# Kernel optimization log

Measured on AMD Instinct MI355X. Metric: run time of the kernel, lower is better.

## Reference

```python
import jax, jax.numpy as jnp
import numpy as np

B, S, D = 4, 8192, 1024
H, DH = 16, 64  # n_heads = d_model // d_head
SCALE = DH ** -0.5


def setup_inputs() -> dict:
    key = jax.random.key(0)
    ks = jax.random.split(key, 4)
    x = jax.random.normal(ks[0], (B, S, D), dtype=jnp.float32)
    Wq = jax.random.normal(ks[1], (D, D), dtype=jnp.float32) * 0.02
    Wkv = jax.random.normal(ks[2], (D, 2 * D), dtype=jnp.float32) * 0.02
    Wlin = jax.random.normal(ks[3], (D, D), dtype=jnp.float32) * 0.02
    blin = jnp.zeros((D,), dtype=jnp.float32)
    return {"x": x, "Wq": Wq, "Wkv": Wkv, "Wlin": Wlin, "blin": blin}


def reference(x, Wq, Wkv, Wlin, blin):
    # Q projection: [B,S,D] -> [B,H,S,DH]
    Q = (x @ Wq).reshape(B, S, H, DH).transpose(0, 2, 1, 3)
    # KV projection: output reshaped per-head as 2*DH then split (matches
    # torch unflatten(-1,(H,2*DH)).chunk(2,-1) interleaving)
    KV = (x @ Wkv).reshape(B, S, H, 2 * DH).transpose(0, 2, 1, 3)  # [B,H,S,2*DH]
    K, V = KV[..., :DH], KV[..., DH:]
    # linear attention: softmax Q over feature dim, K over sequence dim
    Q = jax.nn.softmax(Q, axis=-1) * SCALE
    K = jax.nn.softmax(K, axis=-2)
    # context = K^T @ V : [B,H,DH,DH] (avoids O(S^2) score matrix)
    ctx = jnp.einsum('bhsd,bhse->bhde', K, V)
    out = jnp.einsum('bhsd,bhde->bhse', Q, ctx)  # [B,H,S,DH]
    out = out.transpose(0, 2, 1, 3).reshape(B, S, D)
    return out @ Wlin + blin
```

## Files before the change

### kernel.cpp

```cpp
#include <hip/hip_runtime.h>
#include <cstdint>
#include <cstddef>

typedef unsigned short u16;
typedef unsigned int u32;
typedef __attribute__((ext_vector_type(8))) __bf16 bf16x8;
typedef __attribute__((ext_vector_type(4))) float f32x4;
typedef __attribute__((ext_vector_type(2))) unsigned int u32x2;
typedef __attribute__((ext_vector_type(8))) unsigned short u16x8;
typedef __attribute__((ext_vector_type(4))) unsigned short u16x4;

__device__ __forceinline__ u16 f2bf(float f) {
  union { float f; unsigned u; } v; v.f = f;
  unsigned r = v.u + 0x7fffu + ((v.u >> 16) & 1u);
  return (u16)(r >> 16);
}
__device__ __forceinline__ float bf2f(u16 x) {
  union { float f; unsigned u; } v; v.u = ((unsigned)x) << 16;
  return v.f;
}
__device__ __forceinline__ u32 pk2(float a, float b) {
  union { float f; unsigned u; } x, y; x.f = a; y.f = b;
  unsigned ra = x.u + 0x7fffu + ((x.u >> 16) & 1u);
  unsigned rb = y.u + 0x7fffu + ((y.u >> 16) & 1u);
  return (ra >> 16) | (rb & 0xffff0000u);
}

__device__ __forceinline__ void gll16(const void* g, void* l) {
  __builtin_amdgcn_global_load_lds(
      (const __attribute__((address_space(1))) void*)g,
      (__attribute__((address_space(3))) void*)l, 16, 0, 0);
}

__global__ __launch_bounds__(256) void cvt_x(const float* __restrict__ x,
                                             u16* __restrict__ xb, int n) {
  int i = (blockIdx.x * 256 + threadIdx.x) * 4;
  if (i < n) {
    f32x4 v = __builtin_nontemporal_load((const f32x4*)(x + i));
    u16x4 o = { f2bf(v[0]), f2bf(v[1]), f2bf(v[2]), f2bf(v[3]) };
    *(u16x4*)(xb + i) = o;
  }
}

__global__ __launch_bounds__(256) void build_w3t(const float* __restrict__ Wq,
                                                 const float* __restrict__ Wkv,
                                                 u16* __restrict__ W3t) {
  __shared__ float tile[32][33];
  int bx = blockIdx.x, by = blockIdx.y;
  int tx = threadIdx.x & 31, tyb = threadIdx.x >> 5;
  int n = bx * 32 + tx;
  int u = n & 63;
  int nl = (n & ~63) | ((u & 15) << 2) | (u >> 4);
  const float* src; int scol, sld;
  if (nl < 1024)      { src = Wq;  scol = nl;                                  sld = 1024; }
  else if (nl < 2048) { int m = nl - 1024; src = Wkv; scol = (m >> 6) * 128 + (m & 63);      sld = 2048; }
  else                { int m = nl - 2048; src = Wkv; scol = (m >> 6) * 128 + 64 + (m & 63); sld = 2048; }
#pragma unroll
  for (int i = 0; i < 4; ++i) {
    int k = by * 32 + tyb + i * 8;
    tile[tyb + i * 8][tx] = src[(size_t)k * sld + scol];
  }
  __syncthreads();
#pragma unroll
  for (int i = 0; i < 4; ++i) {
    int n2 = bx * 32 + tyb + i * 8;
    int k2 = by * 32 + tx;
    W3t[(size_t)n2 * 1024 + k2] = f2bf(tile[tx][tyb + i * 8]);
  }
}

template <int MODE>
__global__ __launch_bounds__(512, 2)
void gemm_bt_k(const u16* __restrict__ A, int lda,
               const u16* __restrict__ Bt0, int ldb, int K,
               u16* __restrict__ Lout, int ldc,
               float* __restrict__ Fout,
               float* __restrict__ Zp, const float* __restrict__ bias,
               size_t bstride, int rows_per_batch) {
  __shared__ __align__(16) char sm[131072];
  const int tid  = threadIdx.x;
  const int lane = tid & 63, w = tid >> 6;
  const int wm = w >> 2, wn = w & 3;

  const int nbx = gridDim.x;
  const int nby = gridDim.y;
  const int o = blockIdx.y * nbx + blockIdx.x;
  const int x = o & 7, j = o >> 3;
  const int CM = nby >> 2, CN = nbx >> 1;
  const int jn = j % CN, jm = j / CN;
  const int tileM = ((x >> 1) * CM + jm) * 256;
  const int tileN = ((x & 1) * CN + jn) * 256;

  const u16* Bt = Bt0;
  if (MODE == 2) Bt += (size_t)(tileM / rows_per_batch) * bstride;

  const int r0 = tid >> 3;
  const int pp = (tid & 7) ^ (r0 & 7);
  const u16* gA = A  + (size_t)(tileM + r0) * lda + pp * 8;
  const u16* gB = Bt + (size_t)(tileN + r0) * ldb + pp * 8;
  char* smw = sm + w * 1024;

  const int cl = lane & 15, q = lane >> 4;
  int roA[8], roB[4];
#pragma unroll
  for (int mi = 0; mi < 8; ++mi) roA[mi] = (wm * 128 + mi * 16 + cl) * 128;
#pragma unroll
  for (int ni = 0; ni < 4; ++ni) roB[ni] = (wn * 64 + ni * 16 + cl) * 128;
  const int ck0 = ((0 + q) ^ (cl & 7)) * 16;
  const int ck1 = ((4 + q) ^ (cl & 7)) * 16;

  f32x4 acc[8][4];
#pragma unroll
  for (int i = 0; i < 8; ++i)
#pragma unroll
    for (int j2 = 0; j2 < 4; ++j2) acc[i][j2] = (f32x4){0.f, 0.f, 0.f, 0.f};

  bf16x8 ra[4][2], rb0[2][2], rb1[2][2];

#define FENCE asm volatile("" ::: "memory")
#define STG(ab, g, ld_, bufb, h, kc) do {                                        \
    gll16((g) + (size_t)(h) * 128 * (ld_) + (kc),                                \
          smw + (bufb) + (ab) * 32768 + (h) * 16384);                            \
    gll16((g) + ((size_t)(h) * 128 + 64) * (ld_) + (kc),                         \
          smw + (bufb) + (ab) * 32768 + (h) * 16384 + 8192);                     \
  } while (0)

  const int NT = K >> 6;

  STG(0, gA, lda, 0, 0, 0);
  STG(1, gB, ldb, 0, 0, 0);
  STG(0, gA, lda, 0, 1, 0);
  STG(1, gB, ldb, 0, 1, 0);
  if (NT > 1) {
    STG(0, gA, lda, 65536, 0, 64);
    STG(1, gB, ldb, 65536, 0, 64);
    STG(0, gA, lda, 65536, 1, 64);
    asm volatile("s_waitcnt vmcnt(6)" ::: "memory");
  } else {
    asm volatile("s_waitcnt vmcnt(0)" ::: "memory");
  }
  FENCE; __builtin_amdgcn_s_barrier(); FENCE;

  for (int kt = 0; kt < NT; ++kt) {
    const int bufb  = (kt & 1) << 16;
    const int nbufb = bufb ^ 65536;
    const char* sA = sm + bufb;
    const char* sB = sm + bufb + 32768;

#pragma unroll
    for (int mi = 0; mi < 4; ++mi) {
      ra[mi][0] = *(const bf16x8*)(sA + roA[mi] + ck0);
      ra[mi][1] = *(const bf16x8*)(sA + roA[mi] + ck1);
    }
#pragma unroll
    for (int ni = 0; ni < 2; ++ni) {
      rb0[ni][0] = *(const bf16x8*)(sB + roB[ni] + ck0);
      rb0[ni][1] = *(const bf16x8*)(sB + roB[ni] + ck1);
      rb1[ni][0] = *(const bf16x8*)(sB + roB[2 + ni] + ck0);
      rb1[ni][1] = *(const bf16x8*)(sB + roB[2 + ni] + ck1);
    }
    if (kt + 1 < NT) STG(1, gB, ldb, nbufb, 1, (kt + 1) * 64);
    __builtin_amdgcn_s_setprio(1);
#pragma unroll
    for (int mi = 0; mi < 4; ++mi)
#pragma unroll
      for (int ni = 0; ni < 2; ++ni) {
        acc[mi][ni] = __builtin_amdgcn_mfma_f32_16x16x32_bf16(ra[mi][0], rb0[ni][0], acc[mi][ni], 0, 0, 0);
        acc[mi][ni] = __builtin_amdgcn_mfma_f32_16x16x32_bf16(ra[mi][1], rb0[ni][1], acc[mi][ni], 0, 0, 0);
      }
#pragma unroll
    for (int mi = 0; mi < 4; ++mi)
#pragma unroll
      for (int ni = 0; ni < 2; ++ni) {
        acc[mi][2 + ni] = __builtin_amdgcn_mfma_f32_16x16x32_bf16(ra[mi][0], rb1[ni][0], acc[mi][2 + ni], 0, 0, 0);
        acc[mi][2 + ni] = __builtin_amdgcn_mfma_f32_16x16x32_bf16(ra[mi][1], rb1[ni][1], acc[mi][2 + ni], 0, 0, 0);
      }
    __builtin_amdgcn_s_setprio(0);
    FENCE; __builtin_amdgcn_s_barrier(); FENCE;

#pragma unroll
    for (int mi = 0; mi < 4; ++mi) {
      ra[mi][0] = *(const bf16x8*)(sA + roA[4 + mi] + ck0);
      ra[mi][1] = *(const bf16x8*)(sA + roA[4 + mi] + ck1);
    }
    if (kt + 2 < NT) STG(1, gB, ldb, bufb, 0, (kt + 2) * 64);
    __builtin_amdgcn_s_setprio(1);
#pragma unroll
    for (int mi = 0; mi < 4; ++mi)
#pragma unroll
      for (int ni = 0; ni < 2; ++ni) {
        acc[4 + mi][2 + ni] = __builtin_amdgcn_mfma_f32_16x16x32_bf16(ra[mi][0], rb1[ni][0], acc[4 + mi][2 + ni], 0, 0, 0);
        acc[4 + mi][2 + ni] = __builtin_amdgcn_mfma_f32_16x16x32_bf16(ra[mi][1], rb1[ni][1], acc[4 + mi][2 + ni], 0, 0, 0);
      }
    __builtin_amdgcn_s_setprio(0);
    FENCE; __builtin_amdgcn_s_barrier(); FENCE;

    if (kt + 2 < NT) {
      STG(0, gA, lda, bufb, 0, (kt + 2) * 64);
      STG(0, gA, lda, bufb, 1, (kt + 2) * 64);
    }
    __builtin_amdgcn_s_setprio(1);
#pragma unroll
    for (int mi = 0; mi < 4; ++mi)
#pragma unroll
      for (int ni = 0; ni < 2; ++ni) {
        acc[4 + mi][ni] = __builtin_amdgcn_mfma_f32_16x16x32_bf16(ra[mi][0], rb0[ni][0], acc[4 + mi][ni], 0, 0, 0);
        acc[4 + mi][ni] = __builtin_amdgcn_mfma_f32_16x16x32_bf16(ra[mi][1], rb0[ni][1], acc[4 + mi][ni], 0, 0, 0);
      }
    __builtin_amdgcn_s_setprio(0);
    if (kt + 2 < NT) asm volatile("s_waitcnt vmcnt(6)" ::: "memory");
    else             asm volatile("s_waitcnt vmcnt(0)" ::: "memory");
    FENCE; __builtin_amdgcn_s_barrier(); FENCE;
  }
#undef STG
#undef FENCE

  const int colBase = tileN + wn * 64;
  const int rowBase = tileM + wm * 128;

  if (MODE == 1) {
    if (colBase < 1024) {
#pragma unroll
      for (int mi = 0; mi < 8; ++mi) {
#pragma unroll
        for (int r = 0; r < 4; ++r) {
          float e0 = __expf(acc[mi][0][r]), e1 = __expf(acc[mi][1][r]);
          float e2 = __expf(acc[mi][2][r]), e3 = __expf(acc[mi][3][r]);
          float s = (e0 + e1) + (e2 + e3);
          s += __shfl_xor(s, 1); s += __shfl_xor(s, 2);
          s += __shfl_xor(s, 4); s += __shfl_xor(s, 8);
          float inv = 0.125f / s;
          int row = rowBase + mi * 16 + q * 4 + r;
          u32x2 pv = { pk2(e0 * inv, e1 * inv), pk2(e2 * inv, e3 * inv) };
          __builtin_nontemporal_store(pv, (u32x2*)(Lout + (size_t)row * ldc + colBase + cl * 4));
        }
      }
    } else if (colBase < 2048) {
      float zp0 = 0.f, zp1 = 0.f, zp2 = 0.f, zp3 = 0.f;
      const int b = tileM / rows_per_batch;
#pragma unroll
      for (int mi = 0; mi < 8; ++mi) {
#pragma unroll
        for (int r = 0; r < 4; ++r) {
          float e0 = __expf(acc[mi][0][r]), e1 = __expf(acc[mi][1][r]);
          float e2 = __expf(acc[mi][2][r]), e3 = __expf(acc[mi][3][r]);
          zp0 += e0; zp1 += e1; zp2 += e2; zp3 += e3;
          int row = rowBase + mi * 16 + q * 4 + r;
          u32x2 pv = { pk2(e0, e1), pk2(e2, e3) };
          __builtin_nontemporal_store(pv, (u32x2*)(Lout + (size_t)row * ldc + colBase + cl * 4));
        }
      }
      float zp[4] = { zp0, zp1, zp2, zp3 };
#pragma unroll
      for (int ni = 0; ni < 4; ++ni) {
        float z = zp[ni];
        z += __shfl_xor(z, 16);
        z += __shfl_xor(z, 32);
        if (q == 0) atomicAdd(&Zp[b * 1024 + (colBase - 1024) + cl * 4 + ni], z);
      }
    } else {
#pragma unroll
      for (int mi = 0; mi < 8; ++mi) {
#pragma unroll
        for (int r = 0; r < 4; ++r) {
          int row = rowBase + mi * 16 + q * 4 + r;
          u32x2 pv = { pk2(acc[mi][0][r], acc[mi][1][r]),
                       pk2(acc[mi][2][r], acc[mi][3][r]) };
          __builtin_nontemporal_store(pv, (u32x2*)(Lout + (size_t)row * ldc + colBase + cl * 4));
        }
      }
    }
  } else {
    const float4 bb = *(const float4*)(bias + colBase + cl * 4);
#pragma unroll
    for (int mi = 0; mi < 8; ++mi) {
#pragma unroll
      for (int r = 0; r < 4; ++r) {
        int row = rowBase + mi * 16 + q * 4 + r;
        f32x4 v = { acc[mi][0][r] + bb.x, acc[mi][1][r] + bb.y,
                    acc[mi][2][r] + bb.z, acc[mi][3][r] + bb.w };
        __builtin_nontemporal_store(v, (f32x4*)(Fout + (size_t)row * ldc + colBase + cl * 4));
      }
    }
  }
}

__global__ __launch_bounds__(256) void ctx_mfma(const u16* __restrict__ L,
                                                float* __restrict__ part) {
  __shared__ __align__(16) u16 kvt[4][2][64 * 40];
  const int bh = blockIdx.y, b = bh >> 4, h = bh & 15;
  const int lane = threadIdx.x & 63, w = threadIdx.x >> 6;
  u16* kt = &kvt[w][0][0];
  u16* vt = &kvt[w][1][0];
  const int sl = lane & 31, half = lane >> 5;
  const int cl = lane & 15, q = lane >> 4;

  f32x4 acc[4][4];
#pragma unroll
  for (int i = 0; i < 4; ++i)
#pragma unroll
    for (int j = 0; j < 4; ++j) acc[i][j] = (f32x4){0.f, 0.f, 0.f, 0.f};

  const int sbase0 = blockIdx.x * 1024 + w * 256;
  for (int c = 0; c < 8; ++c) {
    const size_t rowb = ((size_t)b * 8192 + sbase0 + c * 32 + sl) * 3072;
#pragma unroll
    for (int dblk = 0; dblk < 4; ++dblk) {
      int d0 = dblk * 16 + half * 8;
      u16x8 kv = __builtin_nontemporal_load((const u16x8*)(L + rowb + 1024 + h * 64 + d0));
      u16x8 vv = __builtin_nontemporal_load((const u16x8*)(L + rowb + 2048 + h * 64 + d0));
#pragma unroll
      for (int j = 0; j < 8; ++j) {
        kt[(d0 + j) * 40 + sl] = kv[j];
        vt[(d0 + j) * 40 + sl] = vv[j];
      }
    }
    bf16x8 af[4], bfr[4];
#pragma unroll
    for (int mi = 0; mi < 4; ++mi) af[mi]  = *(const bf16x8*)&kt[(mi * 16 + cl) * 40 + q * 8];
#pragma unroll
    for (int ni = 0; ni < 4; ++ni) bfr[ni] = *(const bf16x8*)&vt[(ni * 16 + cl) * 40 + q * 8];
#pragma unroll
    for (int mi = 0; mi < 4; ++mi)
#pragma unroll
      for (int ni = 0; ni < 4; ++ni)
        acc[mi][ni] = __builtin_amdgcn_mfma_f32_16x16x32_bf16(af[mi], bfr[ni], acc[mi][ni], 0, 0, 0);
  }

  const int wslot = blockIdx.x * 4 + w;
  float* pb = part + ((size_t)bh * 32 + wslot) * 4096;
#pragma unroll
  for (int mi = 0; mi < 4; ++mi)
#pragma unroll
    for (int r = 0; r < 4; ++r) {
      float4 v = { acc[mi][0][r], acc[mi][1][r], acc[mi][2][r], acc[mi][3][r] };
      *(float4*)(pb + (mi * 16 + q * 4 + r) * 64 + cl * 4) = v;
    }
}

__global__ __launch_bounds__(256) void norm_ctx(const float* __restrict__ part,
                                                const float* __restrict__ Z,
                                                float* __restrict__ cn) {
  int i = blockIdx.x * 256 + threadIdx.x;
  int bh = i >> 12, rest = i & 4095, d = rest >> 6;
  float s = 0.f;
#pragma unroll
  for (int w = 0; w < 32; ++w) s += part[((size_t)bh * 32 + w) * 4096 + rest];
  cn[i] = s / Z[(bh >> 4) * 1024 + (bh & 15) * 64 + d];
}

__global__ __launch_bounds__(256) void weff_k(const float* __restrict__ cn,
                                              const float* __restrict__ Wlin,
                                              u16* __restrict__ Wt) {
  int bh = blockIdx.y; int b = bh >> 4, h = bh & 15;
  int p = blockIdx.x * 256 + threadIdx.x;
  int up = p & 63;
  int j = (p & ~63) | ((up & 15) << 2) | (up >> 4);
  const float* c = cn + (size_t)bh * 4096;
  float out[64];
#pragma unroll
  for (int d = 0; d < 64; ++d) out[d] = 0.f;
  for (int pe = 0; pe < 64; ++pe) {
    int e = ((pe & 3) << 4) | (pe >> 2);
    float wv = Wlin[(size_t)(h * 64 + e) * 1024 + j];
#pragma unroll
    for (int d = 0; d < 64; ++d) out[d] += c[d * 64 + pe] * wv;
  }
  u16* dst = Wt + ((size_t)b * 1024 + p) * 1024 + h * 64;
#pragma unroll
  for (int d0 = 0; d0 < 64; d0 += 2)
    *(u32*)(dst + d0) = pk2(out[d0], out[d0 + 1]);
}

extern "C" void kernel_launch(void* const* d_in, const int* in_sizes, int n_in,
                              void* d_out, int out_size, void* d_ws, size_t ws_size,
                              hipStream_t stream) {
  const float* x    = (const float*)d_in[0];
  const float* Wq   = (const float*)d_in[1];
  const float* Wkv  = (const float*)d_in[2];
  const float* Wlin = (const float*)d_in[3];
  const float* blin = (const float*)d_in[4];
  float* out = (float*)d_out;
  char* ws = (char*)d_ws;

  u16*   xb   = (u16*)(ws);
  u16*   w3t  = (u16*)(ws + 67108864);
  u16*   L    = (u16*)(ws + 73400320);
  float* Zp   = (float*)(ws + 274726912);
  float* part = (float*)(ws);
  float* cn   = (float*)(ws + 33554432);
  u16*   weff = (u16*)(ws + 34603008);

  hipMemsetAsync(Zp, 0, 16384, stream);

  cvt_x<<<32768, 256, 0, stream>>>(x, xb, 33554432);
  build_w3t<<<dim3(96, 32), 256, 0, stream>>>(Wq, Wkv, w3t);

  gemm_bt_k<1><<<dim3(12, 128), 512, 0, stream>>>(
      xb, 1024, w3t, 1024, 1024, L, 3072, nullptr, Zp, nullptr, (size_t)0, 8192);

  ctx_mfma<<<dim3(8, 64), 256, 0, stream>>>(L, part);
  norm_ctx<<<1024, 256, 0, stream>>>(part, Zp, cn);
  weff_k<<<dim3(4, 64), 256, 0, stream>>>(cn, Wlin, weff);

  gemm_bt_k<2><<<dim3(4, 128), 512, 0, stream>>>(
      L, 3072, weff, 1024, 1024, nullptr, 1024, out, nullptr, blin, (size_t)1048576, 8192);
}
```

Before: 590.3 us.

## Make GEMM kernels persistent with cross-tile prefetch over a flattened K-step loop

Replaces the one-tile-per-block GEMM launch with a persistent grid of 256 blocks. Each block walks a flattened sequence of tiles×K-steps, so global-to-LDS prefetch continues across tile boundaries and the epilogue runs inside the loop when a tile finishes. The aim is to remove per-tile pipeline prologue and drain bubbles and the tail effect of launching many blocks. It also moves the rb1 LDS reads after the first MFMA group to lower register pressure or overlap latency. The cost is extra address arithmetic per step and a larger loop body with the epilogue inlined.

```diff
diff --git a/kernel.cpp b/kernel.cpp
--- a/kernel.cpp
+++ b/kernel.cpp
@@ -69,7 +69,7 @@
   }
 }
 
-template <int MODE>
+template <int MODE, int CN>
 __global__ __launch_bounds__(512, 2)
 void gemm_bt_k(const u16* __restrict__ A, int lda,
                const u16* __restrict__ Bt0, int ldb, int K,
@@ -82,23 +82,31 @@
   const int lane = tid & 63, w = tid >> 6;
   const int wm = w >> 2, wn = w & 3;
 
-  const int nbx = gridDim.x;
-  const int nby = gridDim.y;
-  const int o = blockIdx.y * nbx + blockIdx.x;
-  const int x = o & 7, j = o >> 3;
-  const int CM = nby >> 2, CN = nbx >> 1;
-  const int jn = j % CN, jm = j / CN;
-  const int tileM = ((x >> 1) * CM + jm) * 256;
-  const int tileN = ((x & 1) * CN + jn) * 256;
-
-  const u16* Bt = Bt0;
-  if (MODE == 2) Bt += (size_t)(tileM / rows_per_batch) * bstride;
+  const int p = blockIdx.x, xc = p & 7, sslot = p >> 3;
+
+  auto tileOf = [&](int a, int& tM, int& tN) {
+    int j = a * 32 + sslot;
+    int jm = j / CN, jn = j % CN;
+    tM = ((xc >> 1) * 32 + jm) * 256;
+    tN = ((xc & 1) * CN + jn) * 256;
+  };
 
   const int r0 = tid >> 3;
   const int pp = (tid & 7) ^ (r0 & 7);
-  const u16* gA = A  + (size_t)(tileM + r0) * lda + pp * 8;
-  const u16* gB = Bt + (size_t)(tileN + r0) * ldb + pp * 8;
+  const size_t offA = (size_t)r0 * lda + pp * 8;
+  const size_t offB = (size_t)r0 * ldb + pp * 8;
   char* smw = sm + w * 1024;
+
+  auto baseA = [&](int v) -> const u16* {
+    int tM, tN; tileOf(v >> 4, tM, tN);
+    return A + (size_t)tM * lda + offA + ((v & 15) << 6);
+  };
+  auto baseB = [&](int v) -> const u16* {
+    int tM, tN; tileOf(v >> 4, tM, tN);
+    const u16* b = Bt0;
+    if (MODE == 2) b += (size_t)(tM / rows_per_batch) * bstride;
+    return b + (size_t)tN * ldb + offB + ((v & 15) << 6);
+  };
 
   const int cl = lane & 15, q = lane >> 4;
   int roA[8], roB[4];
@@ -118,31 +126,28 @@
   bf16x8 ra[4][2], rb0[2][2], rb1[2][2];
 
 #define FENCE asm volatile("" ::: "memory")
-#define STG(ab, g, ld_, bufb, h, kc) do {                                        \
-    gll16((g) + (size_t)(h) * 128 * (ld_) + (kc),                                \
-          smw + (bufb) + (ab) * 32768 + (h) * 16384);                            \
-    gll16((g) + ((size_t)(h) * 128 + 64) * (ld_) + (kc),                         \
-          smw + (bufb) + (ab) * 32768 + (h) * 16384 + 8192);                     \
+#define STGA(bufb, h, bp) do {                                                   \
+    gll16((bp) + (size_t)(h) * 128 * lda, smw + (bufb) + (h) * 16384);           \
+    gll16((bp) + ((size_t)(h) * 128 + 64) * lda, smw + (bufb) + (h) * 16384 + 8192); \
   } while (0)
-
-  const int NT = K >> 6;
-
-  STG(0, gA, lda, 0, 0, 0);
-  STG(1, gB, ldb, 0, 0, 0);
-  STG(0, gA, lda, 0, 1, 0);
-  STG(1, gB, ldb, 0, 1, 0);
-  if (NT > 1) {
-    STG(0, gA, lda, 65536, 0, 64);
-    STG(1, gB, ldb, 65536, 0, 64);
-    STG(0, gA, lda, 65536, 1, 64);
+#define STGB(bufb, h, bp) do {                                                   \
+    gll16((bp) + (size_t)(h) * 128 * ldb, smw + (bufb) + 32768 + (h) * 16384);   \
+    gll16((bp) + ((size_t)(h) * 128 + 64) * ldb, smw + (bufb) + 32768 + (h) * 16384 + 8192); \
+  } while (0)
+
+  const int NVT = CN * 16;
+
+  {
+    const u16* a0 = baseA(0); const u16* b0 = baseB(0);
+    STGA(0, 0, a0); STGB(0, 0, b0); STGA(0, 1, a0); STGB(0, 1, b0);
+    const u16* a1 = baseA(1); const u16* b1 = baseB(1);
+    STGA(65536, 0, a1); STGB(65536, 0, b1); STGA(65536, 1, a1);
     asm volatile("s_waitcnt vmcnt(6)" ::: "memory");
-  } else {
-    asm volatile("s_waitcnt vmcnt(0)" ::: "memory");
   }
   FENCE; __builtin_amdgcn_s_barrier(); FENCE;
 
-  for (int kt = 0; kt < NT; ++kt) {
-    const int bufb  = (kt & 1) << 16;
+  for (int v = 0; v < NVT; ++v) {
+    const int bufb  = (v & 1) << 16;
     const int nbufb = bufb ^ 65536;
     const char* sA = sm + bufb;
     const char* sB = sm + bufb + 32768;
@@ -156,10 +161,8 @@
     for (int ni = 0; ni < 2; ++ni) {
       rb0[ni][0] = *(const bf16x8*)(sB + roB[ni] + ck0);
       rb0[ni][1] = *(const bf16x8*)(sB + roB[ni] + ck1);
-      rb1[ni][0] = *(const bf16x8*)(sB + roB[2 + ni] + ck0);
-      rb1[ni][1] = *(const bf16x8*)(sB + roB[2 + ni] + ck1);
-    }
-    if (kt + 1 < NT) STG(1, gB, ldb, nbufb, 1, (kt + 1) * 64);
+    }
+    if (v + 1 < NVT) { const u16* bb = baseB(v + 1); STGB(nbufb, 1, bb); }
     __builtin_amdgcn_s_setprio(1);
 #pragma unroll
     for (int mi = 0; mi < 4; ++mi)
@@ -169,6 +172,11 @@
         acc[mi][ni] = __builtin_amdgcn_mfma_f32_16x16x32_bf16(ra[mi][1], rb0[ni][1], acc[mi][ni], 0, 0, 0);
       }
 #pragma unroll
+    for (int ni = 0; ni < 2; ++ni) {
+      rb1[ni][0] = *(const bf16x8*)(sB + roB[2 + ni] + ck0);
+      rb1[ni][1] = *(const bf16x8*)(sB + roB[2 + ni] + ck1);
+    }
+#pragma unroll
     for (int mi = 0; mi < 4; ++mi)
 #pragma unroll
       for (int ni = 0; ni < 2; ++ni) {
@@ -183,7 +191,7 @@
       ra[mi][0] = *(const bf16x8*)(sA + roA[4 + mi] + ck0);
       ra[mi][1] = *(const bf16x8*)(sA + roA[4 + mi] + ck1);
     }
-    if (kt + 2 < NT) STG(1, gB, ldb, bufb, 0, (kt + 2) * 64);
+    if (v + 2 < NVT) { const u16* bb2 = baseB(v + 2); STGB(bufb, 0, bb2); }
     __builtin_amdgcn_s_setprio(1);
 #pragma unroll
     for (int mi = 0; mi < 4; ++mi)
@@ -195,9 +203,10 @@
     __builtin_amdgcn_s_setprio(0);
     FENCE; __builtin_amdgcn_s_barrier(); FENCE;
 
-    if (kt + 2 < NT) {
-      STG(0, gA, lda, bufb, 0, (kt + 2) * 64);
-      STG(0, gA, lda, bufb, 1, (kt + 2) * 64);
+    if (v + 2 < NVT) {
+      const u16* aa2 = baseA(v + 2);
+      STGA(bufb, 0, aa2);
+      STGA(bufb, 1, aa2);
     }
     __builtin_amdgcn_s_setprio(1);
 #pragma unroll
@@ -208,81 +217,89 @@
         acc[4 + mi][ni] = __builtin_amdgcn_mfma_f32_16x16x32_bf16(ra[mi][1], rb0[ni][1], acc[4 + mi][ni], 0, 0, 0);
       }
     __builtin_amdgcn_s_setprio(0);
-    if (kt + 2 < NT) asm volatile("s_waitcnt vmcnt(6)" ::: "memory");
+    if (v + 2 < NVT) asm volatile("s_waitcnt vmcnt(6)" ::: "memory");
     else             asm volatile("s_waitcnt vmcnt(0)" ::: "memory");
     FENCE; __builtin_amdgcn_s_barrier(); FENCE;
-  }
-#undef STG
+
+    if ((v & 15) == 15) {
+      int tM, tN; tileOf(v >> 4, tM, tN);
+      const int colBase = tN + wn * 64;
+      const int rowBase = tM + wm * 128;
+
+      if (MODE == 1) {
+        if (colBase < 1024) {
+#pragma unroll
+          for (int mi = 0; mi < 8; ++mi) {
+#pragma unroll
+            for (int r = 0; r < 4; ++r) {
+              float e0 = __expf(acc[mi][0][r]), e1 = __expf(acc[mi][1][r]);
+              float e2 = __expf(acc[mi][2][r]), e3 = __expf(acc[mi][3][r]);
+              float s = (e0 + e1) + (e2 + e3);
+              s += __shfl_xor(s, 1); s += __shfl_xor(s, 2);
+              s += __shfl_xor(s, 4); s += __shfl_xor(s, 8);
+              float inv = 0.125f / s;
+              int row = rowBase + mi * 16 + q * 4 + r;
+              u32x2 pv = { pk2(e0 * inv, e1 * inv), pk2(e2 * inv, e3 * inv) };
+              __builtin_nontemporal_store(pv, (u32x2*)(Lout + (size_t)row * ldc + colBase + cl * 4));
+            }
+          }
+        } else if (colBase < 2048) {
+          float zp0 = 0.f, zp1 = 0.f, zp2 = 0.f, zp3 = 0.f;
+          const int b = tM / rows_per_batch;
+#pragma unroll
+          for (int mi = 0; mi < 8; ++mi) {
+#pragma unroll
+            for (int r = 0; r < 4; ++r) {
+              float e0 = __expf(acc[mi][0][r]), e1 = __expf(acc[mi][1][r]);
+              float e2 = __expf(acc[mi][2][r]), e3 = __expf(acc[mi][3][r]);
+              zp0 += e0; zp1 += e1; zp2 += e2; zp3 += e3;
+              int row = rowBase + mi * 16 + q * 4 + r;
+              u32x2 pv = { pk2(e0, e1), pk2(e2, e3) };
+              __builtin_nontemporal_store(pv, (u32x2*)(Lout + (size_t)row * ldc + colBase + cl * 4));
+            }
+          }
+          float zp[4] = { zp0, zp1, zp2, zp3 };
+#pragma unroll
+          for (int ni = 0; ni < 4; ++ni) {
+            float z = zp[ni];
+            z += __shfl_xor(z, 16);
+            z += __shfl_xor(z, 32);
+            if (q == 0) atomicAdd(&Zp[b * 1024 + (colBase - 1024) + cl * 4 + ni], z);
+          }
+        } else {
+#pragma unroll
+          for (int mi = 0; mi < 8; ++mi) {
+#pragma unroll
+            for (int r = 0; r < 4; ++r) {
+              int row = rowBase + mi * 16 + q * 4 + r;
+              u32x2 pv = { pk2(acc[mi][0][r], acc[mi][1][r]),
+                           pk2(acc[mi][2][r], acc[mi][3][r]) };
+              __builtin_nontemporal_store(pv, (u32x2*)(Lout + (size_t)row * ldc + colBase + cl * 4));
+            }
+          }
+        }
+      } else {
+        const float4 bb = *(const float4*)(bias + colBase + cl * 4);
+#pragma unroll
+        for (int mi = 0; mi < 8; ++mi) {
+#pragma unroll
+          for (int r = 0; r < 4; ++r) {
+            int row = rowBase + mi * 16 + q * 4 + r;
+            f32x4 vv = { acc[mi][0][r] + bb.x, acc[mi][1][r] + bb.y,
+                         acc[mi][2][r] + bb.z, acc[mi][3][r] + bb.w };
+            __builtin_nontemporal_store(vv, (f32x4*)(Fout + (size_t)row * ldc + colBase + cl * 4));
+          }
+        }
+      }
+#pragma unroll
+      for (int i = 0; i < 8; ++i)
+#pragma unroll
+        for (int j2 = 0; j2 < 4; ++j2) acc[i][j2] = (f32x4){0.f, 0.f, 0.f, 0.f};
+    }
+  }
+#undef STGA
+#undef STGB
 #undef FENCE
-
-  const int colBase = tileN + wn * 64;
-  const int rowBase = tileM + wm * 128;
-
-  if (MODE == 1) {
-    if (colBase < 1024) {
-#pragma unroll
-      for (int mi = 0; mi < 8; ++mi) {
-#pragma unroll
-        for (int r = 0; r < 4; ++r) {
-          float e0 = __expf(acc[mi][0][r]), e1 = __expf(acc[mi][1][r]);
-          float e2 = __expf(acc[mi][2][r]), e3 = __expf(acc[mi][3][r]);
-          float s = (e0 + e1) + (e2 + e3);
-          s += __shfl_xor(s, 1); s += __shfl_xor(s, 2);
-          s += __shfl_xor(s, 4); s += __shfl_xor(s, 8);
-          float inv = 0.125f / s;
-          int row = rowBase + mi * 16 + q * 4 + r;
-          u32x2 pv = { pk2(e0 * inv, e1 * inv), pk2(e2 * inv, e3 * inv) };
-          __builtin_nontemporal_store(pv, (u32x2*)(Lout + (size_t)row * ldc + colBase + cl * 4));
-        }
-      }
-    } else if (colBase < 2048) {
-      float zp0 = 0.f, zp1 = 0.f, zp2 = 0.f, zp3 = 0.f;
-      const int b = tileM / rows_per_batch;
-#pragma unroll
-      for (int mi = 0; mi < 8; ++mi) {
-#pragma unroll
-        for (int r = 0; r < 4; ++r) {
-          float e0 = __expf(acc[mi][0][r]), e1 = __expf(acc[mi][1][r]);
-          float e2 = __expf(acc[mi][2][r]), e3 = __expf(acc[mi][3][r]);
-          zp0 += e0; zp1 += e1; zp2 += e2; zp3 += e3;
-          int row = rowBase + mi * 16 + q * 4 + r;
-          u32x2 pv = { pk2(e0, e1), pk2(e2, e3) };
-          __builtin_nontemporal_store(pv, (u32x2*)(Lout + (size_t)row * ldc + colBase + cl * 4));
-        }
-      }
-      float zp[4] = { zp0, zp1, zp2, zp3 };
-#pragma unroll
-      for (int ni = 0; ni < 4; ++ni) {
-        float z = zp[ni];
-        z += __shfl_xor(z, 16);
-        z += __shfl_xor(z, 32);
-        if (q == 0) atomicAdd(&Zp[b * 1024 + (colBase - 1024) + cl * 4 + ni], z);
-      }
-    } else {
-#pragma unroll
-      for (int mi = 0; mi < 8; ++mi) {
-#pragma unroll
-        for (int r = 0; r < 4; ++r) {
-          int row = rowBase + mi * 16 + q * 4 + r;
-          u32x2 pv = { pk2(acc[mi][0][r], acc[mi][1][r]),
-                       pk2(acc[mi][2][r], acc[mi][3][r]) };
-          __builtin_nontemporal_store(pv, (u32x2*)(Lout + (size_t)row * ldc + colBase + cl * 4));
-        }
-      }
-    }
-  } else {
-    const float4 bb = *(const float4*)(bias + colBase + cl * 4);
-#pragma unroll
-    for (int mi = 0; mi < 8; ++mi) {
-#pragma unroll
-      for (int r = 0; r < 4; ++r) {
-        int row = rowBase + mi * 16 + q * 4 + r;
-        f32x4 v = { acc[mi][0][r] + bb.x, acc[mi][1][r] + bb.y,
-                    acc[mi][2][r] + bb.z, acc[mi][3][r] + bb.w };
-        __builtin_nontemporal_store(v, (f32x4*)(Fout + (size_t)row * ldc + colBase + cl * 4));
-      }
-    }
-  }
 }
 
 __global__ __launch_bounds__(256) void ctx_mfma(const u16* __restrict__ L,
@@ -396,13 +413,13 @@
   cvt_x<<<32768, 256, 0, stream>>>(x, xb, 33554432);
   build_w3t<<<dim3(96, 32), 256, 0, stream>>>(Wq, Wkv, w3t);
 
-  gemm_bt_k<1><<<dim3(12, 128), 512, 0, stream>>>(
+  gemm_bt_k<1, 6><<<256, 512, 0, stream>>>(
       xb, 1024, w3t, 1024, 1024, L, 3072, nullptr, Zp, nullptr, (size_t)0, 8192);
 
   ctx_mfma<<<dim3(8, 64), 256, 0, stream>>>(L, part);
   norm_ctx<<<1024, 256, 0, stream>>>(part, Zp, cn);
   weff_k<<<dim3(4, 64), 256, 0, stream>>>(cn, Wlin, weff);
 
-  gemm_bt_k<2><<<dim3(4, 128), 512, 0, stream>>>(
+  gemm_bt_k<2, 2><<<256, 512, 0, stream>>>(
       L, 3072, weff, 1024, 1024, nullptr, 1024, out, nullptr, blin, (size_t)1048576, 8192);
 }
```

New measurement: 586.5 us. No clear change (-0.6%).
